# Performance work log

Measured on AMD Instinct MI355X. Metric: run time of the kernel, lower is better.

The kernel has to match this reference:

```python
import jax, jax.numpy as jnp
import numpy as np

B, S, HID = 2, 2048, 2048
NH, HD = 16, 128
EPS = 1e-5
ROPE_BASE = 10000.0


def setup_inputs() -> dict:
    key = jax.random.key(0)
    k1, k2, k3 = jax.random.split(key, 3)
    std = 1.0 / np.sqrt(HID)
    x = jax.random.normal(k1, (B, S, HID), jnp.float32)
    w_in = jax.random.truncated_normal(k2, -3.0, 3.0, (3 * NH * HD, HID), jnp.float32) * std
    std_o = std / np.sqrt(2.0)  # layer_id = 0 -> std / sqrt(2*(0+1))
    w_out = jax.random.truncated_normal(k3, -3.0, 3.0, (HID, NH * HD), jnp.float32) * std_o
    q_norm_w = jnp.ones((NH * HD,), jnp.float32)
    k_norm_w = jnp.ones((NH * HD,), jnp.float32)
    return {"x": x, "w_in": w_in, "w_out": w_out, "q_norm_w": q_norm_w, "k_norm_w": k_norm_w}


def _rms_norm(x, w, eps=EPS):
    ms = jnp.mean(x * x, axis=-1, keepdims=True)
    return x * jax.lax.rsqrt(ms + eps) * w


def _rope(x, offset=0):
    # x: [B, S, NH, HD]; rotate-half convention
    half = HD // 2
    inv_freq = 1.0 / (ROPE_BASE ** (jnp.arange(half, dtype=jnp.float32) / half))
    pos = jnp.arange(x.shape[1], dtype=jnp.float32) + offset
    ang = pos[:, None] * inv_freq                      # [S, half]
    cos = jnp.cos(ang)[None, :, None, :]
    sin = jnp.sin(ang)[None, :, None, :]
    x1, x2 = jnp.split(x, 2, axis=-1)
    return jnp.concatenate([x1 * cos - x2 * sin, x2 * cos + x1 * sin], axis=-1)


def reference(x, w_in, w_out, q_norm_w, k_norm_w):
    b, s, _ = x.shape
    qkv = jnp.einsum('bsh,oh->bso', x, w_in)           # [B, S, 3*NH*HD]
    q, k, v = jnp.split(qkv, 3, axis=-1)
    # qk-norm over the flat (NH*HD) axis, as in the torch module
    q = _rms_norm(q, q_norm_w)
    k = _rms_norm(k, k_norm_w)
    q = q.reshape(b, s, NH, HD)
    k = k.reshape(b, s, NH, HD)
    v = v.reshape(b, s, NH, HD)
    q = _rope(q)
    k = _rope(k)
    scale = 1.0 / np.sqrt(HD)
    scores = jnp.einsum('bqhd,bkhd->bhqk', q, k) * scale
    causal = jnp.tril(jnp.ones((s, s), dtype=bool))
    scores = jnp.where(causal[None, None, :, :], scores, jnp.finfo(scores.dtype).min)
    probs = jax.nn.softmax(scores, axis=-1)
    out = jnp.einsum('bhqk,bkhd->bqhd', probs, v).reshape(b, s, NH * HD)
    return jnp.einsum('bso,ho->bsh', out, w_out)
```

## Files before the change

kernel.cpp:

```cpp
#include <hip/hip_runtime.h>
#include <hip/hip_bf16.h>
#include <math.h>

#define B_   2
#define S_   2048
#define HID_ 2048
#define NH_  16
#define HD_  128
#define QKV_ (3 * NH_ * HD_)
#define EPS_ 1e-5f

typedef __bf16 bf16x8 __attribute__((ext_vector_type(8)));
typedef __bf16 bf16x4 __attribute__((ext_vector_type(4)));
typedef __bf16 bf16x2 __attribute__((ext_vector_type(2)));
typedef float  f32x4  __attribute__((ext_vector_type(4)));

__global__ __launch_bounds__(256) void cast3_f32_bf16(
    const float* __restrict__ a, __bf16* __restrict__ ao, int na4,
    const float* __restrict__ b, __bf16* __restrict__ bo, int nb4,
    const float* __restrict__ c, __bf16* __restrict__ co, int nc4) {
    int j = blockIdx.x * 256 + threadIdx.x;
    const float* src;
    __bf16* dst;
    if (j < na4) {
        src = a; dst = ao;
    } else {
        j -= na4;
        if (j < nb4) {
            src = b; dst = bo;
        } else {
            j -= nb4;
            if (j >= nc4) return;
            src = c; dst = co;
        }
    }
    float4 v = reinterpret_cast<const float4*>(src)[j];
    bf16x4 o = {(__bf16)v.x, (__bf16)v.y, (__bf16)v.z, (__bf16)v.w};
    reinterpret_cast<bf16x4*>(dst)[j] = o;
}

__device__ __forceinline__ void gload_lds16(const __bf16* g, __bf16* l) {
    __builtin_amdgcn_global_load_lds(
        (const __attribute__((address_space(1))) void*)g,
        (__attribute__((address_space(3))) void*)l, 16, 0, 0);
}

#define BARR  __builtin_amdgcn_s_barrier()
#define LGKM0 asm volatile("s_waitcnt lgkmcnt(0)" ::: "memory")
#define FENCE asm volatile("" ::: "memory")

__device__ __forceinline__ void read_a4x(const __bf16* bc, int wm, int lrow,
                                         int quad, int swz, int qq,
                                         bf16x8 (&af)[2][2]) {
#pragma unroll
    for (int i2 = 0; i2 < 2; ++i2)
#pragma unroll
        for (int kk = 0; kk < 2; ++kk)
            af[i2][kk] = *reinterpret_cast<const bf16x8*>(
                &bc[(wm * 128 + (qq * 2 + i2) * 16 + lrow) * 64 +
                    (((kk * 4 + quad) ^ swz) << 3)]);
}

__device__ __forceinline__ void read_b6(const __bf16* bc, int wn, int lrow,
                                        int quad, int swz,
                                        bf16x8 (&bf)[3][2]) {
#pragma unroll
    for (int j = 0; j < 3; ++j)
#pragma unroll
        for (int kk = 0; kk < 2; ++kk)
            bf[j][kk] = *reinterpret_cast<const bf16x8*>(
                &bc[16384 + (wn * 48 + j * 16 + lrow) * 64 +
                    (((kk * 4 + quad) ^ swz) << 3)]);
}

__device__ __forceinline__ void mfma12(int qq, const bf16x8 (&af)[2][2],
                                       const bf16x8 (&bf)[3][2],
                                       f32x4 (&acc)[8][3]) {
    __builtin_amdgcn_s_setprio(1);
#pragma unroll
    for (int i2 = 0; i2 < 2; ++i2)
#pragma unroll
        for (int j = 0; j < 3; ++j)
#pragma unroll
            for (int kk = 0; kk < 2; ++kk)
                acc[qq * 2 + i2][j] = __builtin_amdgcn_mfma_f32_16x16x32_bf16(
                    af[i2][kk], bf[j][kk], acc[qq * 2 + i2][j], 0, 0, 0);
    __builtin_amdgcn_s_setprio(0);
}

__global__ __launch_bounds__(512, 2) void gemm1_192(
    const __bf16* __restrict__ A, const __bf16* __restrict__ Bm,
    __bf16* __restrict__ C, int M, int N, int K) {
    __shared__ __bf16 lds[2][28672];

    const int tid  = threadIdx.x;
    const int w    = tid >> 6;
    const int lane = tid & 63;
    const int lrow = lane & 15;
    const int quad = lane >> 4;
    const int wm   = w >> 2;
    const int wn   = w & 3;
    const int swz  = lrow & 7;

    const int chunk = (int)gridDim.x >> 3;
    const int flat  = (int)blockIdx.x;
    const int vid   = (flat & 7) * chunk + (flat >> 3);
    const int m0 = (vid & 15) * 256;
    const int n0 = (vid >> 4) * 192;

    const int lr = lane >> 3;
    const int lg = lane & 7;
    const size_t K64 = (size_t)K * 64;
    const __bf16* pA = A  + (size_t)(m0 + w * 8 + lr) * K + ((lg ^ lr) << 3);
    const __bf16* pB = Bm + (size_t)(n0 + w * 8 + lr) * K + ((lg ^ lr) << 3);

#define STA(c, tt, dst) gload_lds16(pA + (size_t)(c) * K64 + (size_t)(tt) * 64, \
                                    (dst) + (c) * 4096 + w * 512)
#define STB(c, tt, dst) gload_lds16(pB + (size_t)(c) * K64 + (size_t)(tt) * 64, \
                                    (dst) + 16384 + (c) * 4096 + w * 512)

    f32x4 acc[8][3] = {};
    bf16x8 af[2][2], bf[3][2];

    {
        __bf16* d = &lds[0][0];
        STB(0, 0, d); STB(1, 0, d); STB(2, 0, d);
        FENCE;
        STA(0, 0, d); STA(2, 0, d);
        FENCE;
        STA(1, 0, d); STA(3, 0, d);
    }
    asm volatile("s_waitcnt vmcnt(2)" ::: "memory");
    BARR;

    const int nt = K >> 6;
    for (int t = 0; t < nt - 1; ++t) {
        __bf16* bc = &lds[t & 1][0];
        __bf16* bn = &lds[(t & 1) ^ 1][0];
        const int tn = t + 1;
        read_a4x(bc, wm, lrow, quad, swz, 0, af);
        read_b6(bc, wn, lrow, quad, swz, bf);
        STB(0, tn, bn); STB(1, tn, bn);
        BARR; LGKM0;
        mfma12(0, af, bf, acc);
        BARR;
        read_a4x(bc, wm, lrow, quad, swz, 1, af);
        STB(2, tn, bn);
        BARR; LGKM0;
        mfma12(1, af, bf, acc);
        asm volatile("s_waitcnt vmcnt(3)" ::: "memory");
        BARR;
        read_a4x(bc, wm, lrow, quad, swz, 2, af);
        STA(0, tn, bn); STA(2, tn, bn);
        BARR; LGKM0;
        mfma12(2, af, bf, acc);
        BARR;
        read_a4x(bc, wm, lrow, quad, swz, 3, af);
        STA(1, tn, bn); STA(3, tn, bn);
        BARR; LGKM0;
        mfma12(3, af, bf, acc);
        asm volatile("s_waitcnt vmcnt(2)" ::: "memory");
        BARR;
    }
    {
        __bf16* bc = &lds[(nt - 1) & 1][0];
        read_a4x(bc, wm, lrow, quad, swz, 0, af);
        read_b6(bc, wn, lrow, quad, swz, bf);
        BARR; LGKM0;
        mfma12(0, af, bf, acc);
        BARR;
        read_a4x(bc, wm, lrow, quad, swz, 1, af);
        BARR; LGKM0;
        mfma12(1, af, bf, acc);
        asm volatile("s_waitcnt vmcnt(0)" ::: "memory");
        BARR;
        read_a4x(bc, wm, lrow, quad, swz, 2, af);
        BARR; LGKM0;
        mfma12(2, af, bf, acc);
        BARR;
        read_a4x(bc, wm, lrow, quad, swz, 3, af);
        BARR; LGKM0;
        mfma12(3, af, bf, acc);
    }
#undef STA
#undef STB

#pragma unroll
    for (int mf = 0; mf < 8; ++mf) {
#pragma unroll
        for (int r = 0; r < 4; ++r) {
            int row = m0 + wm * 128 + mf * 16 + quad * 4 + r;
            size_t cb = (size_t)row * N + n0 + wn * 48 + lrow;
#pragma unroll
            for (int j = 0; j < 3; ++j)
                C[cb + j * 16] = (__bf16)acc[mf][j][r];
        }
    }
}

__device__ __forceinline__ void stage_tile6(
    const __bf16* pA, const __bf16* pB, __bf16* buf, int w, int K) {
#pragma unroll
    for (int s = 0; s < 2; ++s)
        gload_lds16(pA + (size_t)s * 64 * K, buf + s * 4096 + w * 512);
#pragma unroll
    for (int s = 0; s < 4; ++s)
        gload_lds16(pB + (size_t)s * 64 * K, buf + 8192 + s * 4096 + w * 512);
}

template <typename OutT>
__global__ __launch_bounds__(512, 2) void gemm_bt_8ph(
    const __bf16* __restrict__ A, const __bf16* __restrict__ Bm,
    OutT* __restrict__ C, int M, int N, int K) {
    __shared__ __bf16 lds[3][24576];

    const int tid  = threadIdx.x;
    const int w    = tid >> 6;
    const int lane = tid & 63;
    const int lrow = lane & 15;
    const int quad = lane >> 4;
    const int wm   = w >> 2;
    const int wn   = w & 3;

    const int chunk = (int)gridDim.x >> 3;
    const int flat  = (int)blockIdx.x;
    const int vid   = (flat & 7) * chunk + (flat >> 3);
    const int by    = vid & 31;
    const int bx    = vid >> 5;
    const int m0 = by * 128;
    const int n0 = bx * 256;

    const int lr = lane >> 3;
    const int lg = lane & 7;
    const __bf16* pA = A  + (size_t)(m0 + w * 8 + lr) * K + ((lg ^ lr) << 3);
    const __bf16* pB = Bm + (size_t)(n0 + w * 8 + lr) * K + ((lg ^ lr) << 3);

    const int nt = K >> 6;
    f32x4 acc[4][4] = {};

    stage_tile6(pA, pB, &lds[0][0], w, K);
    stage_tile6(pA + 64, pB + 64, &lds[1][0], w, K);

    int cur = 0;
    for (int t = 0; t < nt; ++t) {
        __bf16* bufc = &lds[cur][0];
        int nxt = cur + 2; if (nxt >= 3) nxt -= 3;
        if (t + 2 < nt) {
            stage_tile6(pA + (size_t)(t + 2) * 64, pB + (size_t)(t + 2) * 64,
                        &lds[nxt][0], w, K);
            asm volatile("s_waitcnt vmcnt(12)" ::: "memory");
        } else if (t + 1 < nt) {
            asm volatile("s_waitcnt vmcnt(6)" ::: "memory");
        } else {
            asm volatile("s_waitcnt vmcnt(0)" ::: "memory");
        }
        BARR;
        FENCE;

#pragma unroll
        for (int q = 0; q < 2; ++q) {
            bf16x8 af[2][2], bfv[4][2];
#pragma unroll
            for (int i = 0; i < 2; ++i)
#pragma unroll
                for (int kk = 0; kk < 2; ++kk)
                    af[i][kk] = *reinterpret_cast<const bf16x8*>(
                        &bufc[(wm * 64 + (q * 2 + i) * 16 + lrow) * 64 +
                              (((kk * 4 + quad) ^ (lrow & 7)) << 3)]);
#pragma unroll
            for (int j = 0; j < 4; ++j)
#pragma unroll
                for (int kk = 0; kk < 2; ++kk)
                    bfv[j][kk] = *reinterpret_cast<const bf16x8*>(
                        &bufc[8192 + (wn * 64 + j * 16 + lrow) * 64 +
                              (((kk * 4 + quad) ^ (lrow & 7)) << 3)]);
            BARR;
            FENCE;
            __builtin_amdgcn_s_setprio(1);
#pragma unroll
            for (int i = 0; i < 2; ++i)
#pragma unroll
                for (int j = 0; j < 4; ++j)
#pragma unroll
                    for (int kk = 0; kk < 2; ++kk)
                        acc[q * 2 + i][j] =
                            __builtin_amdgcn_mfma_f32_16x16x32_bf16(
                                af[i][kk], bfv[j][kk], acc[q * 2 + i][j],
                                0, 0, 0);
            __builtin_amdgcn_s_setprio(0);
        }
        BARR;
        FENCE;
        cur = (cur == 2) ? 0 : cur + 1;
    }

#pragma unroll
    for (int mi = 0; mi < 4; ++mi) {
#pragma unroll
        for (int r = 0; r < 4; ++r) {
            int row = m0 + wm * 64 + mi * 16 + quad * 4 + r;
            size_t basec = (size_t)row * N + n0 + wn * 64 + lrow;
#pragma unroll
            for (int nj = 0; nj < 4; ++nj)
                C[basec + nj * 16] = (OutT)acc[mi][nj][r];
        }
    }
}

__global__ __launch_bounds__(256) void normrope_kernel(
    __bf16* __restrict__ qkv, const float* __restrict__ qw,
    const float* __restrict__ kw) {
    const int row = blockIdx.x;
    const int sel = blockIdx.y;
    const int pos = row & (S_ - 1);
    __bf16* p = qkv + (size_t)row * QKV_ + sel * 2048;
    const float* w = sel ? kw : qw;

    __shared__ float buf[2048];
    __shared__ float red[4];
    const int tid = threadIdx.x;
    const int e   = tid * 8;

    bf16x8 t = *reinterpret_cast<const bf16x8*>(&p[e]);
    float xs[8];
    float ss = 0.f;
#pragma unroll
    for (int u = 0; u < 8; ++u) {
        xs[u] = (float)t[u];
        buf[e + u] = xs[u];
        ss += xs[u] * xs[u];
    }
#pragma unroll
    for (int off = 32; off > 0; off >>= 1) ss += __shfl_xor(ss, off, 64);
    if ((tid & 63) == 0) red[tid >> 6] = ss;
    __syncthreads();
    float total = red[0] + red[1] + red[2] + red[3];
    float scale = rsqrtf(total * (1.f / 2048.f) + EPS_);

    const float kfreq2 = -0.20762050593046f;
    const int jbase = e & 63;
    const bool first = (e & 127) < 64;
    const int ep = e ^ 64;

    float ps[8], ws[8], pw[8];
#pragma unroll
    for (int u = 0; u < 8; ++u) ps[u] = buf[ep + u];
    float4 w0 = *reinterpret_cast<const float4*>(&w[e]);
    float4 w1 = *reinterpret_cast<const float4*>(&w[e + 4]);
    float4 p0 = *reinterpret_cast<const float4*>(&w[ep]);
    float4 p1 = *reinterpret_cast<const float4*>(&w[ep + 4]);
    ws[0]=w0.x; ws[1]=w0.y; ws[2]=w0.z; ws[3]=w0.w;
    ws[4]=w1.x; ws[5]=w1.y; ws[6]=w1.z; ws[7]=w1.w;
    pw[0]=p0.x; pw[1]=p0.y; pw[2]=p0.z; pw[3]=p0.w;
    pw[4]=p1.x; pw[5]=p1.y; pw[6]=p1.z; pw[7]=p1.w;

    bf16x8 o8;
#pragma unroll
    for (int u = 0; u < 8; ++u) {
        float inv_freq = exp2f((float)(jbase + u) * kfreq2);
        float ang = (float)pos * inv_freq;
        float sn = __sinf(ang);
        float cs = __cosf(ang);
        float a  = xs[u] * scale * ws[u];
        float bb = ps[u] * scale * pw[u];
        float o  = first ? (a * cs - bb * sn) : (a * cs + bb * sn);
        o8[u] = (__bf16)o;
    }
    *reinterpret_cast<bf16x8*>(&p[e]) = o8;
}

#define VTP 36

__global__ __launch_bounds__(512, 4) void attn_mfma(
    const __bf16* __restrict__ qkv, __bf16* __restrict__ aout) {
    const int flat = (int)blockIdx.x;
    const int vid  = (flat & 7) * 64 + (flat >> 3);
    const int bh   = vid >> 4;
    const int qt   = 15 - (vid & 15);
    const int b    = bh >> 4;
    const int h    = bh & (NH_ - 1);
    const int q0   = qt * 128;
    const int tid  = threadIdx.x;
    const int w    = tid >> 6;
    const int lane = tid & 63;
    const int lrow = lane & 15;
    const int quad = lane >> 4;

    __shared__ __bf16 Ks[2][4][32 * 32];
    __shared__ __bf16 Vt[2][128 * VTP];
    __shared__ __bf16 Pb[8][16 * VTP];

    const size_t base = (size_t)(b * S_) * QKV_ + (size_t)h * HD_;
    const int qrow = q0 + w * 16 + lrow;

    bf16x8 qf[4];
#pragma unroll
    for (int kc = 0; kc < 4; ++kc)
        qf[kc] = *reinterpret_cast<const bf16x8*>(
            &qkv[base + (size_t)qrow * QKV_ + kc * 32 + quad * 8]);

    f32x4 o[8] = {};
    float lpart = 0.f;

    const int ktmax_w   = 4 * qt + (w >> 1);
    const int ktmax_blk = 4 * qt + 3;
    const float sl2 = 0.12751743671f;
    const int kgq = (quad ^ ((lrow >> 1) & 3)) * 8;

    const __bf16* kg0 = qkv + base + 2048 +
                        (size_t)((w & 1) * 16 + (lane >> 2)) * QKV_ +
                        (w >> 1) * 32 + (((lane & 3) ^ ((lane >> 3) & 3)) << 3);
    const int g  = tid >> 4;
    const int kp = tid & 15;
    const __bf16* vg0 = qkv + base + 4096 + (size_t)(kp * 2) * QKV_ + g * 8;

    gload_lds16(kg0, &Ks[0][w >> 1][(w & 1) * 512]);
    bf16x8 v0 = {}, v1 = {};
    if (tid < 256) {
        v0 = *reinterpret_cast<const bf16x8*>(vg0);
        v1 = *reinterpret_cast<const bf16x8*>(vg0 + QKV_);
    }

    for (int kt = 0; kt <= ktmax_blk; ++kt) {
        const int buf = kt & 1;
        if (tid < 256) {
#pragma unroll
            for (int u = 0; u < 8; ++u) {
                bf16x2 pr = {v0[u], v1[u]};
                *reinterpret_cast<bf16x2*>(
                    &Vt[buf][(g * 8 + u) * VTP + kp * 2]) = pr;
            }
        }
        __syncthreads();
        if (kt < ktmax_blk) {
            const __bf16* kg = kg0 + (size_t)(kt + 1) * 32 * QKV_;
            gload_lds16(kg, &Ks[buf ^ 1][w >> 1][(w & 1) * 512]);
            if (tid < 256) {
                const __bf16* vg = vg0 + (size_t)(kt + 1) * 32 * QKV_;
                v0 = *reinterpret_cast<const bf16x8*>(vg);
                v1 = *reinterpret_cast<const bf16x8*>(vg + QKV_);
            }
        }
        if (kt <= ktmax_w) {
            f32x4 sc[2] = {};
            __builtin_amdgcn_s_setprio(1);
#pragma unroll
            for (int kc = 0; kc < 4; ++kc) {
                bf16x8 kf0 = *reinterpret_cast<const bf16x8*>(
                    &Ks[buf][kc][lrow * 32 + kgq]);
                bf16x8 kf1 = *reinterpret_cast<const bf16x8*>(
                    &Ks[buf][kc][(16 + lrow) * 32 + kgq]);
                sc[0] = __builtin_amdgcn_mfma_f32_16x16x32_bf16(
                    kf0, qf[kc], sc[0], 0, 0, 0);
                sc[1] = __builtin_amdgcn_mfma_f32_16x16x32_bf16(
                    kf1, qf[kc], sc[1], 0, 0, 0);
            }
            __builtin_amdgcn_s_setprio(0);
            const bool diag = (kt == ktmax_w);
            float p[2][4];
#pragma unroll
            for (int m2 = 0; m2 < 2; ++m2)
#pragma unroll
                for (int r = 0; r < 4; ++r) {
                    float s = sc[m2][r] * sl2 - 32.f;
                    if (diag && kt * 32 + m2 * 16 + quad * 4 + r > qrow)
                        s = -1e30f;
                    p[m2][r] = exp2f(s);
                    lpart += p[m2][r];
                }
#pragma unroll
            for (int m2 = 0; m2 < 2; ++m2) {
                bf16x4 pb = {(__bf16)p[m2][0], (__bf16)p[m2][1],
                             (__bf16)p[m2][2], (__bf16)p[m2][3]};
                *reinterpret_cast<bf16x4*>(
                    &Pb[w][lrow * VTP + m2 * 16 + quad * 4]) = pb;
            }
            bf16x8 pf = *reinterpret_cast<const bf16x8*>(
                &Pb[w][lrow * VTP + quad * 8]);
            __builtin_amdgcn_s_setprio(1);
#pragma unroll
            for (int dt = 0; dt < 8; ++dt) {
                bf16x8 vf = *reinterpret_cast<const bf16x8*>(
                    &Vt[buf][(dt * 16 + lrow) * VTP + quad * 8]);
                o[dt] = __builtin_amdgcn_mfma_f32_16x16x32_bf16(
                    vf, pf, o[dt], 0, 0, 0);
            }
            __builtin_amdgcn_s_setprio(0);
        }
    }

    lpart += __shfl_xor(lpart, 16, 64);
    lpart += __shfl_xor(lpart, 32, 64);
    const float invl = 1.f / lpart;
    const size_t orow = (size_t)(b * S_ + qrow) * (NH_ * HD_) + (size_t)h * HD_;
#pragma unroll
    for (int dt = 0; dt < 8; ++dt) {
        bf16x4 ov = {(__bf16)(o[dt][0] * invl), (__bf16)(o[dt][1] * invl),
                     (__bf16)(o[dt][2] * invl), (__bf16)(o[dt][3] * invl)};
        *reinterpret_cast<bf16x4*>(&aout[orow + dt * 16 + quad * 4]) = ov;
    }
}

extern "C" void kernel_launch(void* const* d_in, const int* in_sizes, int n_in,
                              void* d_out, int out_size, void* d_ws,
                              size_t ws_size, hipStream_t stream) {
    const float* x     = (const float*)d_in[0];
    const float* w_in  = (const float*)d_in[1];
    const float* w_out = (const float*)d_in[2];
    const float* qw    = (const float*)d_in[3];
    const float* kw    = (const float*)d_in[4];
    float* out = (float*)d_out;

    const int M = B_ * S_;
    char* ws = (char*)d_ws;
    __bf16* qkv_b   = (__bf16*)(ws);
    __bf16* w_out_b = (__bf16*)(ws + (size_t)50331648);
    __bf16* x_b     = (__bf16*)(ws + (size_t)58720256);
    __bf16* attn_b  = x_b;
    __bf16* w_in_b  = (__bf16*)(ws + (size_t)75497472);

    dim3 blk(256);

    {
        const int na4 = (M * HID_) / 4;
        const int nb4 = (QKV_ * HID_) / 4;
        const int nc4 = (HID_ * NH_ * HD_) / 4;
        const int tot = na4 + nb4 + nc4;
        cast3_f32_bf16<<<dim3((tot + 255) / 256), blk, 0, stream>>>(
            x, x_b, na4, w_in, w_in_b, nb4, w_out, w_out_b, nc4);
    }

    gemm1_192<<<dim3((M / 256) * (QKV_ / 192)), dim3(512), 0, stream>>>(
        x_b, w_in_b, qkv_b, M, QKV_, HID_);
    normrope_kernel<<<dim3(M, 2), blk, 0, stream>>>(qkv_b, qw, kw);
    attn_mfma<<<dim3((S_ / 128) * B_ * NH_), dim3(512), 0, stream>>>(
        qkv_b, attn_b);
    gemm_bt_8ph<float><<<dim3((M / 128) * (HID_ / 256)), dim3(512), 0,
                         stream>>>(attn_b, w_out_b, out, M, HID_, NH_ * HD_);
}
```

Baseline: 383.6 us.

## Deepen attention K/V prefetch to two tiles ahead with triple-buffered K

Moves the attention K loads to a three-slot LDS ring and keeps two register sets for V, so global loads are issued two KV tiles ahead instead of one. The plain barrier is replaced with explicit vmcnt/lgkmcnt waits plus barrier macros, which lets one tile's load stay in flight while the current tile is computed. The aim is to hide more global-memory latency. The cost is extra LDS and registers, which may lower occupancy, and the hand-written waitcnt logic is easy to get wrong.

```diff
diff --git a/kernel.cpp b/kernel.cpp
--- a/kernel.cpp
+++ b/kernel.cpp
@@ -386,7 +386,7 @@
     const int lrow = lane & 15;
     const int quad = lane >> 4;
 
-    __shared__ __bf16 Ks[2][4][32 * 32];
+    __shared__ __bf16 Ks[3][4][32 * 32];
     __shared__ __bf16 Vt[2][128 * VTP];
     __shared__ __bf16 Pb[8][16 * VTP];
 
@@ -413,32 +413,61 @@
     const int g  = tid >> 4;
     const int kp = tid & 15;
     const __bf16* vg0 = qkv + base + 4096 + (size_t)(kp * 2) * QKV_ + g * 8;
-
-    gload_lds16(kg0, &Ks[0][w >> 1][(w & 1) * 512]);
-    bf16x8 v0 = {}, v1 = {};
+    const int kslot = (w >> 1) * 1024 + (w & 1) * 512;
+
+    bf16x8 vA0 = {}, vA1 = {}, vB0 = {}, vB1 = {};
+    gload_lds16(kg0, &Ks[0][0][kslot]);
     if (tid < 256) {
-        v0 = *reinterpret_cast<const bf16x8*>(vg0);
-        v1 = *reinterpret_cast<const bf16x8*>(vg0 + QKV_);
-    }
-
+        vA0 = *reinterpret_cast<const bf16x8*>(vg0);
+        vA1 = *reinterpret_cast<const bf16x8*>(vg0 + QKV_);
+    }
+    FENCE;
+    gload_lds16(kg0 + (size_t)32 * QKV_, &Ks[1][0][kslot]);
+    if (tid < 256) {
+        vB0 = *reinterpret_cast<const bf16x8*>(vg0 + (size_t)32 * QKV_);
+        vB1 = *reinterpret_cast<const bf16x8*>(vg0 + (size_t)33 * QKV_);
+    }
+
+    int bk = 0;
     for (int kt = 0; kt <= ktmax_blk; ++kt) {
-        const int buf = kt & 1;
+        const int bufv = kt & 1;
         if (tid < 256) {
-#pragma unroll
-            for (int u = 0; u < 8; ++u) {
-                bf16x2 pr = {v0[u], v1[u]};
-                *reinterpret_cast<bf16x2*>(
-                    &Vt[buf][(g * 8 + u) * VTP + kp * 2]) = pr;
+            if (bufv == 0) {
+#pragma unroll
+                for (int u = 0; u < 8; ++u) {
+                    bf16x2 pr = {vA0[u], vA1[u]};
+                    *reinterpret_cast<bf16x2*>(
+                        &Vt[0][(g * 8 + u) * VTP + kp * 2]) = pr;
+                }
+            } else {
+#pragma unroll
+                for (int u = 0; u < 8; ++u) {
+                    bf16x2 pr = {vB0[u], vB1[u]};
+                    *reinterpret_cast<bf16x2*>(
+                        &Vt[1][(g * 8 + u) * VTP + kp * 2]) = pr;
+                }
             }
-        }
-        __syncthreads();
-        if (kt < ktmax_blk) {
-            const __bf16* kg = kg0 + (size_t)(kt + 1) * 32 * QKV_;
-            gload_lds16(kg, &Ks[buf ^ 1][w >> 1][(w & 1) * 512]);
+        } else {
+            if (kt < ktmax_blk)
+                asm volatile("s_waitcnt vmcnt(1)" ::: "memory");
+            else
+                asm volatile("s_waitcnt vmcnt(0)" ::: "memory");
+        }
+        LGKM0;
+        BARR;
+        FENCE;
+        if (kt + 2 <= ktmax_blk) {
+            int bk2 = bk + 2; if (bk2 >= 3) bk2 -= 3;
+            gload_lds16(kg0 + (size_t)(kt + 2) * 32 * QKV_, &Ks[bk2][0][kslot]);
             if (tid < 256) {
-                const __bf16* vg = vg0 + (size_t)(kt + 1) * 32 * QKV_;
-                v0 = *reinterpret_cast<const bf16x8*>(vg);
-                v1 = *reinterpret_cast<const bf16x8*>(vg + QKV_);
+                const __bf16* vg = vg0 + (size_t)(kt + 2) * 32 * QKV_;
+                if (bufv == 0) {
+                    vA0 = *reinterpret_cast<const bf16x8*>(vg);
+                    vA1 = *reinterpret_cast<const bf16x8*>(vg + QKV_);
+                } else {
+                    vB0 = *reinterpret_cast<const bf16x8*>(vg);
+                    vB1 = *reinterpret_cast<const bf16x8*>(vg + QKV_);
+                }
             }
         }
         if (kt <= ktmax_w) {
@@ -447,9 +476,9 @@
 #pragma unroll
             for (int kc = 0; kc < 4; ++kc) {
                 bf16x8 kf0 = *reinterpret_cast<const bf16x8*>(
-                    &Ks[buf][kc][lrow * 32 + kgq]);
+                    &Ks[bk][kc][lrow * 32 + kgq]);
                 bf16x8 kf1 = *reinterpret_cast<const bf16x8*>(
-                    &Ks[buf][kc][(16 + lrow) * 32 + kgq]);
+                    &Ks[bk][kc][(16 + lrow) * 32 + kgq]);
                 sc[0] = __builtin_amdgcn_mfma_f32_16x16x32_bf16(
                     kf0, qf[kc], sc[0], 0, 0, 0);
                 sc[1] = __builtin_amdgcn_mfma_f32_16x16x32_bf16(
@@ -481,12 +510,13 @@
 #pragma unroll
             for (int dt = 0; dt < 8; ++dt) {
                 bf16x8 vf = *reinterpret_cast<const bf16x8*>(
-                    &Vt[buf][(dt * 16 + lrow) * VTP + quad * 8]);
+                    &Vt[bufv][(dt * 16 + lrow) * VTP + quad * 8]);
                 o[dt] = __builtin_amdgcn_mfma_f32_16x16x32_bf16(
                     vf, pf, o[dt], 0, 0, 0);
             }
             __builtin_amdgcn_s_setprio(0);
         }
+        bk = (bk == 2) ? 0 : bk + 1;
     }
 
     lpart += __shfl_xor(lpart, 16, 64);
```

Measured after the change: 391.7 us. 1.02x slower.

## Widen attention KV tile from 32 to 64 keys per iteration

Applied to the files above, without the earlier changes.

The attention kernel now processes 64 keys per loop iteration instead of 32. This halves the number of barriers and loop iterations, and all 512 threads now take part in the V transpose load instead of half. It raises LDS use per block (larger K and Vt buffers), which may lower occupancy at the 4-blocks launch bound. Causal waste on the diagonal tile also grows.

```diff
diff --git a/kernel.cpp b/kernel.cpp
--- a/kernel.cpp
+++ b/kernel.cpp
@@ -369,7 +369,8 @@
     *reinterpret_cast<bf16x8*>(&p[e]) = o8;
 }
 
-#define VTP 36
+#define VTP 68
+#define PBP 36
 
 __global__ __launch_bounds__(512, 4) void attn_mfma(
     const __bf16* __restrict__ qkv, __bf16* __restrict__ aout) {
@@ -386,9 +387,9 @@
     const int lrow = lane & 15;
     const int quad = lane >> 4;
 
-    __shared__ __bf16 Ks[2][4][32 * 32];
+    __shared__ __bf16 Ks[2][4][64 * 32];
     __shared__ __bf16 Vt[2][128 * VTP];
-    __shared__ __bf16 Pb[8][16 * VTP];
+    __shared__ __bf16 Pb[8][16 * PBP];
 
     const size_t base = (size_t)(b * S_) * QKV_ + (size_t)h * HD_;
     const int qrow = q0 + w * 16 + lrow;
@@ -402,90 +403,90 @@
     f32x4 o[8] = {};
     float lpart = 0.f;
 
-    const int ktmax_w   = 4 * qt + (w >> 1);
-    const int ktmax_blk = 4 * qt + 3;
+    const int ktmax_w   = 2 * qt + (w >> 2);
+    const int ktmax_blk = 2 * qt + 1;
     const float sl2 = 0.12751743671f;
     const int kgq = (quad ^ ((lrow >> 1) & 3)) * 8;
 
     const __bf16* kg0 = qkv + base + 2048 +
-                        (size_t)((w & 1) * 16 + (lane >> 2)) * QKV_ +
+                        (size_t)((w & 1) * 32 + (lane >> 2)) * QKV_ +
                         (w >> 1) * 32 + (((lane & 3) ^ ((lane >> 3) & 3)) << 3);
-    const int g  = tid >> 4;
-    const int kp = tid & 15;
+    const int kslot = (w & 1) * 1024;
+    const int g  = tid >> 5;
+    const int kp = tid & 31;
     const __bf16* vg0 = qkv + base + 4096 + (size_t)(kp * 2) * QKV_ + g * 8;
 
-    gload_lds16(kg0, &Ks[0][w >> 1][(w & 1) * 512]);
-    bf16x8 v0 = {}, v1 = {};
-    if (tid < 256) {
-        v0 = *reinterpret_cast<const bf16x8*>(vg0);
-        v1 = *reinterpret_cast<const bf16x8*>(vg0 + QKV_);
-    }
+    gload_lds16(kg0, &Ks[0][w >> 1][kslot]);
+    gload_lds16(kg0 + (size_t)16 * QKV_, &Ks[0][w >> 1][kslot + 512]);
+    bf16x8 v0 = *reinterpret_cast<const bf16x8*>(vg0);
+    bf16x8 v1 = *reinterpret_cast<const bf16x8*>(vg0 + QKV_);
 
     for (int kt = 0; kt <= ktmax_blk; ++kt) {
         const int buf = kt & 1;
-        if (tid < 256) {
-#pragma unroll
-            for (int u = 0; u < 8; ++u) {
-                bf16x2 pr = {v0[u], v1[u]};
-                *reinterpret_cast<bf16x2*>(
-                    &Vt[buf][(g * 8 + u) * VTP + kp * 2]) = pr;
-            }
+#pragma unroll
+        for (int u = 0; u < 8; ++u) {
+            bf16x2 pr = {v0[u], v1[u]};
+            *reinterpret_cast<bf16x2*>(&Vt[buf][(g * 8 + u) * VTP + kp * 2]) =
+                pr;
         }
         __syncthreads();
         if (kt < ktmax_blk) {
-            const __bf16* kg = kg0 + (size_t)(kt + 1) * 32 * QKV_;
-            gload_lds16(kg, &Ks[buf ^ 1][w >> 1][(w & 1) * 512]);
-            if (tid < 256) {
-                const __bf16* vg = vg0 + (size_t)(kt + 1) * 32 * QKV_;
-                v0 = *reinterpret_cast<const bf16x8*>(vg);
-                v1 = *reinterpret_cast<const bf16x8*>(vg + QKV_);
-            }
+            const __bf16* kg = kg0 + (size_t)(kt + 1) * 64 * QKV_;
+            gload_lds16(kg, &Ks[buf ^ 1][w >> 1][kslot]);
+            gload_lds16(kg + (size_t)16 * QKV_, &Ks[buf ^ 1][w >> 1][kslot + 512]);
+            const __bf16* vg = vg0 + (size_t)(kt + 1) * 64 * QKV_;
+            v0 = *reinterpret_cast<const bf16x8*>(vg);
+            v1 = *reinterpret_cast<const bf16x8*>(vg + QKV_);
         }
         if (kt <= ktmax_w) {
-            f32x4 sc[2] = {};
+            f32x4 sc[4] = {};
             __builtin_amdgcn_s_setprio(1);
 #pragma unroll
             for (int kc = 0; kc < 4; ++kc) {
-                bf16x8 kf0 = *reinterpret_cast<const bf16x8*>(
-                    &Ks[buf][kc][lrow * 32 + kgq]);
-                bf16x8 kf1 = *reinterpret_cast<const bf16x8*>(
-                    &Ks[buf][kc][(16 + lrow) * 32 + kgq]);
-                sc[0] = __builtin_amdgcn_mfma_f32_16x16x32_bf16(
-                    kf0, qf[kc], sc[0], 0, 0, 0);
-                sc[1] = __builtin_amdgcn_mfma_f32_16x16x32_bf16(
-                    kf1, qf[kc], sc[1], 0, 0, 0);
+#pragma unroll
+                for (int kg2 = 0; kg2 < 4; ++kg2) {
+                    bf16x8 kf = *reinterpret_cast<const bf16x8*>(
+                        &Ks[buf][kc][(kg2 * 16 + lrow) * 32 + kgq]);
+                    sc[kg2] = __builtin_amdgcn_mfma_f32_16x16x32_bf16(
+                        kf, qf[kc], sc[kg2], 0, 0, 0);
+                }
             }
             __builtin_amdgcn_s_setprio(0);
             const bool diag = (kt == ktmax_w);
-            float p[2][4];
-#pragma unroll
-            for (int m2 = 0; m2 < 2; ++m2)
+            float p[4][4];
+#pragma unroll
+            for (int kg2 = 0; kg2 < 4; ++kg2)
 #pragma unroll
                 for (int r = 0; r < 4; ++r) {
-                    float s = sc[m2][r] * sl2 - 32.f;
-                    if (diag && kt * 32 + m2 * 16 + quad * 4 + r > qrow)
+                    float s = sc[kg2][r] * sl2 - 32.f;
+                    if (diag &&
+                        kt * 64 + kg2 * 16 + quad * 4 + r > qrow)
                         s = -1e30f;
-                    p[m2][r] = exp2f(s);
-                    lpart += p[m2][r];
+                    p[kg2][r] = exp2f(s);
+                    lpart += p[kg2][r];
                 }
 #pragma unroll
-            for (int m2 = 0; m2 < 2; ++m2) {
-                bf16x4 pb = {(__bf16)p[m2][0], (__bf16)p[m2][1],
-                             (__bf16)p[m2][2], (__bf16)p[m2][3]};
-                *reinterpret_cast<bf16x4*>(
-                    &Pb[w][lrow * VTP + m2 * 16 + quad * 4]) = pb;
+            for (int hh = 0; hh < 2; ++hh) {
+#pragma unroll
+                for (int m2 = 0; m2 < 2; ++m2) {
+                    const int kg2 = hh * 2 + m2;
+                    bf16x4 pb = {(__bf16)p[kg2][0], (__bf16)p[kg2][1],
+                                 (__bf16)p[kg2][2], (__bf16)p[kg2][3]};
+                    *reinterpret_cast<bf16x4*>(
+                        &Pb[w][lrow * PBP + m2 * 16 + quad * 4]) = pb;
+                }
+                bf16x8 pf = *reinterpret_cast<const bf16x8*>(
+                    &Pb[w][lrow * PBP + quad * 8]);
+                __builtin_amdgcn_s_setprio(1);
+#pragma unroll
+                for (int dt = 0; dt < 8; ++dt) {
+                    bf16x8 vf = *reinterpret_cast<const bf16x8*>(
+                        &Vt[buf][(dt * 16 + lrow) * VTP + hh * 32 + quad * 8]);
+                    o[dt] = __builtin_amdgcn_mfma_f32_16x16x32_bf16(
+                        vf, pf, o[dt], 0, 0, 0);
+                }
+                __builtin_amdgcn_s_setprio(0);
             }
-            bf16x8 pf = *reinterpret_cast<const bf16x8*>(
-                &Pb[w][lrow * VTP + quad * 8]);
-            __builtin_amdgcn_s_setprio(1);
-#pragma unroll
-            for (int dt = 0; dt < 8; ++dt) {
-                bf16x8 vf = *reinterpret_cast<const bf16x8*>(
-                    &Vt[buf][(dt * 16 + lrow) * VTP + quad * 8]);
-                o[dt] = __builtin_amdgcn_mfma_f32_16x16x32_bf16(
-                    vf, pf, o[dt], 0, 0, 0);
-            }
-            __builtin_amdgcn_s_setprio(0);
         }
     }
 
```

Result: no change. 385.1 us (+0.4%).
